# Optimization experiments

Measured on AMD Instinct MI355X. Metric: run time of the kernel, lower is better.

The kernel has to match this reference:

```python
import jax, jax.numpy as jnp
import numpy as np

B, C, H, W = 16, 512, 64, 64
R = 8
CP = C // R  # inner channel dim C' = 64


def setup_inputs() -> dict:
    key = jax.random.key(0)
    ks = jax.random.split(key, 10)
    s_in = 1.0 / np.sqrt(C)
    s_cp = 1.0 / np.sqrt(CP)
    return {
        "x": jax.random.normal(ks[0], (B, C, H, W), dtype=jnp.float32),
        "wq": jax.random.uniform(ks[1], (CP, C), jnp.float32, -s_in, s_in),
        "bq": jax.random.uniform(ks[2], (CP,), jnp.float32, -s_in, s_in),
        "wk": jax.random.uniform(ks[3], (CP, C), jnp.float32, -s_in, s_in),
        "bk": jax.random.uniform(ks[4], (CP,), jnp.float32, -s_in, s_in),
        "wv": jax.random.uniform(ks[5], (CP, C), jnp.float32, -s_in, s_in),
        "bv": jax.random.uniform(ks[6], (CP,), jnp.float32, -s_in, s_in),
        "wo": jax.random.uniform(ks[7], (C, CP), jnp.float32, -s_cp, s_cp),
        "bo": jax.random.uniform(ks[8], (C,), jnp.float32, -s_cp, s_cp),
        # torch init is gamma=0 (output==x, zero grads to convs); use small
        # nonzero value so the reference exercises the full graph.
        "gamma": jax.random.normal(ks[9], (1,), dtype=jnp.float32) * 0.1,
    }


def reference(x, wq, bq, wk, bk, wv, bv, wo, bo, gamma):
    b, c, h, w = x.shape
    n = h * w
    xf = x.reshape(b, c, n)  # flatten spatial -> (B, C, N)
    # 1x1 convs == channel matmuls
    q = jnp.einsum("oc,bcn->bon", wq, xf) + bq[:, None]  # (B, C', N)
    k = jnp.einsum("oc,bcn->bon", wk, xf) + bk[:, None]  # (B, C', N)
    v = jnp.einsum("oc,bcn->bon", wv, xf) + bv[:, None]  # (B, C', N)
    # energy = bmm(key (B,C',N), query^T (B,N,C')) -> (B, C', C')
    energy = jnp.einsum("bin,bjn->bij", k, q)
    attention = jax.nn.softmax(energy, axis=-1)  # (B, C', C')
    out = jnp.einsum("bij,bjn->bin", attention, v)  # (B, C', N)
    out = jnp.einsum("co,bon->bcn", wo, out) + bo[:, None]  # (B, C, N)
    out = out.reshape(b, c, h, w)
    return gamma * out + x
```

## Files before the change

kernel.cpp:

```cpp
#include <hip/hip_runtime.h>
#include <hip/hip_bf16.h>


#define NN 4096
#define CIN 512
#define CPD 64

typedef short s8v __attribute__((ext_vector_type(8)));
typedef float f4v __attribute__((ext_vector_type(4)));

__device__ __forceinline__ unsigned short f2bf(float f) {
    union { float f; unsigned int u; } c; c.f = f;
    unsigned int r = c.u + 0x7FFFu + ((c.u >> 16) & 1u);
    return (unsigned short)(r >> 16);
}

__global__ __launch_bounds__(512, 2) void k_qkv(
    const float* __restrict__ x,
    const float* __restrict__ wq, const float* __restrict__ bq,
    const float* __restrict__ wk, const float* __restrict__ bk,
    const float* __restrict__ wv, const float* __restrict__ bv,
    unsigned short* __restrict__ q, unsigned short* __restrict__ k,
    unsigned short* __restrict__ vt)
{
    const int nb = blockIdx.x, b = blockIdx.y;
    const int t = threadIdx.x;
    const int wv_ = t >> 6, L = t & 63, quad = L >> 4, l15 = L & 15;
    const int swz = (l15 & 7) * 8;

    __shared__ unsigned short wl[3][64 * 128];

    const float* wptr[3] = { wq, wk, wv };

    f4v acc[3][4][2];
    #pragma unroll
    for (int p = 0; p < 3; ++p)
        #pragma unroll
        for (int ot = 0; ot < 4; ++ot)
            #pragma unroll
            for (int nn = 0; nn < 2; ++nn) acc[p][ot][nn] = (f4v){0.f,0.f,0.f,0.f};

    const int n_col0 = nb * 256 + wv_ * 32 + l15;
    const size_t xbase = (size_t)b * CIN * NN;

    for (int cc = 0; cc < 4; ++cc) {
        __syncthreads();
        {
            const int o   = t & 63;
            const int c16 = (t >> 6) * 16;
            const int osw = (o & 7) * 8;
            #pragma unroll
            for (int p = 0; p < 3; ++p) {
                const float* wp = wptr[p] + (size_t)o * CIN + cc * 128 + c16;
                unsigned short tmp[16];
                #pragma unroll
                for (int f = 0; f < 4; ++f) {
                    float4 v = *(const float4*)(wp + f * 4);
                    tmp[f*4+0] = f2bf(v.x); tmp[f*4+1] = f2bf(v.y);
                    tmp[f*4+2] = f2bf(v.z); tmp[f*4+3] = f2bf(v.w);
                }
                #pragma unroll
                for (int u = 0; u < 2; ++u)
                    *(uint4*)&wl[p][o * 128 + ((c16 + u * 8) ^ osw)] =
                        *(const uint4*)&tmp[u * 8];
            }
        }
        __syncthreads();

        #pragma unroll
        for (int ksl = 0; ksl < 4; ++ksl) {
            const int c = cc * 128 + ksl * 32 + quad * 8;
            float bx0[8], bx1[8];
            #pragma unroll
            for (int j = 0; j < 8; ++j) {
                const float* xc = x + xbase + (size_t)(c + j) * NN + n_col0;
                bx0[j] = xc[0];
                bx1[j] = xc[16];
            }
            s8v bf0, bf1;
            #pragma unroll
            for (int j = 0; j < 8; ++j) {
                bf0[j] = (short)f2bf(bx0[j]);
                bf1[j] = (short)f2bf(bx1[j]);
            }
            const int cfrag = (ksl * 32 + quad * 8) ^ swz;
            #pragma unroll
            for (int p = 0; p < 3; ++p)
                #pragma unroll
                for (int ot = 0; ot < 4; ++ot) {
                    s8v af = *(const s8v*)&wl[p][(ot * 16 + l15) * 128 + cfrag];
                    acc[p][ot][0] = __builtin_amdgcn_mfma_f32_16x16x32_bf16(
                        af, bf0, acc[p][ot][0], 0, 0, 0);
                    acc[p][ot][1] = __builtin_amdgcn_mfma_f32_16x16x32_bf16(
                        af, bf1, acc[p][ot][1], 0, 0, 0);
                }
        }
    }

    const float* biasp[3] = { bq, bk, bv };
    #pragma unroll
    for (int p = 0; p < 2; ++p) {
        unsigned short* outp = ((p == 0) ? q : k) + (size_t)b * CPD * NN;
        #pragma unroll
        for (int ot = 0; ot < 4; ++ot) {
            float4 b4 = *(const float4*)(biasp[p] + ot * 16 + quad * 4);
            const float bsv[4] = { b4.x, b4.y, b4.z, b4.w };
            #pragma unroll
            for (int nn = 0; nn < 2; ++nn) {
                const int n = n_col0 + nn * 16;
                #pragma unroll
                for (int r = 0; r < 4; ++r) {
                    int o = ot * 16 + quad * 4 + r;
                    outp[(size_t)o * NN + n] = f2bf(acc[p][ot][nn][r] + bsv[r]);
                }
            }
        }
    }
    {
        unsigned short* vtb = vt + (size_t)b * NN * CPD;
        #pragma unroll
        for (int ot = 0; ot < 4; ++ot) {
            float4 b4 = *(const float4*)(bv + ot * 16 + quad * 4);
            const float bsv[4] = { b4.x, b4.y, b4.z, b4.w };
            #pragma unroll
            for (int nn = 0; nn < 2; ++nn) {
                const int n = n_col0 + nn * 16;
                unsigned short tmp[4];
                #pragma unroll
                for (int r = 0; r < 4; ++r) tmp[r] = f2bf(acc[2][ot][nn][r] + bsv[r]);
                *(uint2*)(vtb + (size_t)n * CPD + ot * 16 + quad * 4) = *(const uint2*)tmp;
            }
        }
    }
}

__global__ __launch_bounds__(256) void k_energy(
    const unsigned short* __restrict__ q, const unsigned short* __restrict__ k,
    float* __restrict__ epart)
{
    const int s = blockIdx.x;
    const int b = blockIdx.y;
    const int t = threadIdx.x;
    const int wv_ = t >> 6, L = t & 63, quad = L >> 4, l15 = L & 15;
    const unsigned short* kb = k + (size_t)b * CPD * NN;
    const unsigned short* qb = q + (size_t)b * CPD * NN;

    __shared__ float red[64 * 65];

    f4v acc[4][4];
    #pragma unroll
    for (int a = 0; a < 4; ++a)
        #pragma unroll
        for (int d = 0; d < 4; ++d) acc[a][d] = (f4v){0.f,0.f,0.f,0.f};

    const int nbase = s * 512 + wv_ * 128;
    #pragma unroll
    for (int ks = 0; ks < 4; ++ks) {
        const int n = nbase + ks * 32 + quad * 8;
        s8v af[4], bf_[4];
        #pragma unroll
        for (int it = 0; it < 4; ++it)
            af[it] = *(const s8v*)(kb + (size_t)(it * 16 + l15) * NN + n);
        #pragma unroll
        for (int jt = 0; jt < 4; ++jt)
            bf_[jt] = *(const s8v*)(qb + (size_t)(jt * 16 + l15) * NN + n);
        #pragma unroll
        for (int it = 0; it < 4; ++it)
            #pragma unroll
            for (int jt = 0; jt < 4; ++jt)
                acc[it][jt] = __builtin_amdgcn_mfma_f32_16x16x32_bf16(
                    af[it], bf_[jt], acc[it][jt], 0, 0, 0);
    }

    for (int idx = t; idx < 64 * 65; idx += 256) red[idx] = 0.f;
    __syncthreads();
    #pragma unroll
    for (int it = 0; it < 4; ++it)
        #pragma unroll
        for (int jt = 0; jt < 4; ++jt)
            #pragma unroll
            for (int r = 0; r < 4; ++r)
                atomicAdd(&red[(it * 16 + quad * 4 + r) * 65 + jt * 16 + l15],
                          acc[it][jt][r]);
    __syncthreads();
    float* ep = epart + ((size_t)b * 8 + s) * 4096;
    for (int idx = t; idx < 4096; idx += 256)
        ep[idx] = red[(idx >> 6) * 65 + (idx & 63)];
}

__global__ __launch_bounds__(64) void k_softmax(
    const float* __restrict__ epart, unsigned short* __restrict__ attn)
{
    const int i = blockIdx.x;
    const int b = blockIdx.y;
    const int j = threadIdx.x;
    float s = 0.f;
    #pragma unroll
    for (int sp = 0; sp < 8; ++sp)
        s += epart[((size_t)b * 8 + sp) * 4096 + i * 64 + j];
    float m = s;
    #pragma unroll
    for (int off = 32; off; off >>= 1) m = fmaxf(m, __shfl_xor(m, off));
    float e = __expf(s - m);
    float tot = e;
    #pragma unroll
    for (int off = 32; off; off >>= 1) tot += __shfl_xor(tot, off);
    attn[(size_t)b * 4096 + i * 64 + j] = f2bf(e / tot);
}

__global__ __launch_bounds__(256) void k_avout(
    const unsigned short* __restrict__ vt, const unsigned short* __restrict__ attn,
    const float* __restrict__ wo, const float* __restrict__ bo,
    const float* __restrict__ gamma, const float* __restrict__ x,
    float* __restrict__ out)
{
    const int nb = blockIdx.x, b = blockIdx.y;
    const int t = threadIdx.x;
    const int wv_ = t >> 6, L = t & 63, quad = L >> 4, l15 = L & 15;
    const int swz = (l15 & 7) * 8;

    __shared__ unsigned short wol[512 * 64];
    __shared__ unsigned short avl[128 * 64];

    {
        const int i16 = (t & 3) * 16;
        #pragma unroll
        for (int pass = 0; pass < 8; ++pass) {
            const int c = (t >> 2) + pass * 64;
            const int csw = (c & 7) * 8;
            const float* wp = wo + (size_t)c * CPD + i16;
            unsigned short tmp[16];
            #pragma unroll
            for (int f = 0; f < 4; ++f) {
                float4 v = *(const float4*)(wp + f * 4);
                tmp[f*4+0] = f2bf(v.x); tmp[f*4+1] = f2bf(v.y);
                tmp[f*4+2] = f2bf(v.z); tmp[f*4+3] = f2bf(v.w);
            }
            #pragma unroll
            for (int u = 0; u < 2; ++u)
                *(uint4*)&wol[c * 64 + ((i16 + u * 8) ^ csw)] = *(const uint4*)&tmp[u*8];
        }
    }

    {
        const unsigned short* ab  = attn + (size_t)b * 4096;
        const unsigned short* vtb = vt + (size_t)b * NN * CPD;
        const int n0 = nb * 128;
        f4v acc1[4][2];
        #pragma unroll
        for (int a = 0; a < 4; ++a)
            #pragma unroll
            for (int d = 0; d < 2; ++d) acc1[a][d] = (f4v){0.f,0.f,0.f,0.f};
        #pragma unroll
        for (int ks = 0; ks < 2; ++ks) {
            const int j = ks * 32 + quad * 8;
            s8v af[4], bf_[2];
            #pragma unroll
            for (int it = 0; it < 4; ++it)
                af[it] = *(const s8v*)(ab + (size_t)(it * 16 + l15) * 64 + j);
            #pragma unroll
            for (int nn = 0; nn < 2; ++nn)
                bf_[nn] = *(const s8v*)(vtb +
                    (size_t)(n0 + wv_ * 32 + nn * 16 + l15) * CPD + j);
            #pragma unroll
            for (int it = 0; it < 4; ++it)
                #pragma unroll
                for (int nn = 0; nn < 2; ++nn)
                    acc1[it][nn] = __builtin_amdgcn_mfma_f32_16x16x32_bf16(
                        af[it], bf_[nn], acc1[it][nn], 0, 0, 0);
        }
        #pragma unroll
        for (int it = 0; it < 4; ++it)
            #pragma unroll
            for (int nn = 0; nn < 2; ++nn) {
                const int nloc = wv_ * 32 + nn * 16 + l15;
                unsigned short tmp[4];
                #pragma unroll
                for (int r = 0; r < 4; ++r) tmp[r] = f2bf(acc1[it][nn][r]);
                *(uint2*)&avl[nloc * 64 + ((it * 16 + quad * 4) ^ swz)] =
                    *(const uint2*)tmp;
            }
    }
    __syncthreads();

    const float g = gamma[0];
    const int n0 = nb * 128;
    for (int cb = 0; cb < 8; ++cb) {
        f4v acc2[2][4];
        #pragma unroll
        for (int a = 0; a < 2; ++a)
            #pragma unroll
            for (int d = 0; d < 4; ++d) acc2[a][d] = (f4v){0.f,0.f,0.f,0.f};
        #pragma unroll
        for (int ks = 0; ks < 2; ++ks) {
            const int ic = (ks * 32 + quad * 8) ^ swz;
            s8v af2[2], bf2[4];
            #pragma unroll
            for (int nt = 0; nt < 2; ++nt)
                af2[nt] = *(const s8v*)&avl[(wv_ * 32 + nt * 16 + l15) * 64 + ic];
            #pragma unroll
            for (int ct = 0; ct < 4; ++ct)
                bf2[ct] = *(const s8v*)&wol[(cb * 64 + ct * 16 + l15) * 64 + ic];
            #pragma unroll
            for (int nt = 0; nt < 2; ++nt)
                #pragma unroll
                for (int ct = 0; ct < 4; ++ct)
                    acc2[nt][ct] = __builtin_amdgcn_mfma_f32_16x16x32_bf16(
                        af2[nt], bf2[ct], acc2[nt][ct], 0, 0, 0);
        }
        #pragma unroll
        for (int nt = 0; nt < 2; ++nt)
            #pragma unroll
            for (int ct = 0; ct < 4; ++ct) {
                const int c = cb * 64 + ct * 16 + l15;
                const float bs = bo[c];
                const int nbase = n0 + wv_ * 32 + nt * 16 + quad * 4;
                const size_t idx = ((size_t)b * CIN + c) * NN + nbase;
                float4 xr = *(const float4*)(x + idx);
                float4 r4;
                r4.x = g * (acc2[nt][ct][0] + bs) + xr.x;
                r4.y = g * (acc2[nt][ct][1] + bs) + xr.y;
                r4.z = g * (acc2[nt][ct][2] + bs) + xr.z;
                r4.w = g * (acc2[nt][ct][3] + bs) + xr.w;
                *(float4*)(out + idx) = r4;
            }
    }
}

extern "C" void kernel_launch(void* const* d_in, const int* in_sizes, int n_in,
                              void* d_out, int out_size, void* d_ws, size_t ws_size,
                              hipStream_t stream) {
    const float* x  = (const float*)d_in[0];
    const float* wq = (const float*)d_in[1];
    const float* bq = (const float*)d_in[2];
    const float* wk = (const float*)d_in[3];
    const float* bk = (const float*)d_in[4];
    const float* wv = (const float*)d_in[5];
    const float* bv = (const float*)d_in[6];
    const float* wo = (const float*)d_in[7];
    const float* bo = (const float*)d_in[8];
    const float* gm = (const float*)d_in[9];
    float* out = (float*)d_out;

    char* wsb = (char*)d_ws;
    unsigned short* q     = (unsigned short*)wsb;
    unsigned short* k     = (unsigned short*)(wsb + 8388608);
    unsigned short* vt    = (unsigned short*)(wsb + 16777216);
    float*          epart = (float*)(wsb + 25165824);
    unsigned short* attn  = (unsigned short*)(wsb + 27262976);

    k_qkv<<<dim3(16, 16), 512, 0, stream>>>(x, wq, bq, wk, bk, wv, bv, q, k, vt);
    k_energy<<<dim3(8, 16), 256, 0, stream>>>(q, k, epart);
    k_softmax<<<dim3(64, 16), 64, 0, stream>>>(epart, attn);
    k_avout<<<dim3(32, 16), 256, 0, stream>>>(vt, attn, wo, bo, gm, x, out);
}
```

Baseline: 341.0 us.

## Pre-convert weights to bf16 once and drop LDS staging in GEMM kernels

Adds a prep kernel that converts wq/wk/wv/wo to bf16 in workspace, so k_qkv and k_avout read bf16 weights straight from global/L2 and no longer convert and stage them in shared memory. k_qkv uses 256-thread blocks covering 128 columns with all 12 output tiles per wave, which doubles the grid and removes the block-level syncs. k_energy uses more, smaller blocks and writes per-wave partials with no LDS atomics, and softmax now sums 64 partials. The cost is an extra launch, more partial-sum traffic (a 16MB epart), and uncoalesced weight fragment loads from global memory.

```diff
diff --git a/kernel.cpp b/kernel.cpp
--- a/kernel.cpp
+++ b/kernel.cpp
@@ -1,5 +1,4 @@
 #include <hip/hip_runtime.h>
-#include <hip/hip_bf16.h>
 
 
 #define NN 4096
@@ -8,243 +7,203 @@
 
 typedef short s8v __attribute__((ext_vector_type(8)));
 typedef float f4v __attribute__((ext_vector_type(4)));
-
-__device__ __forceinline__ unsigned short f2bf(float f) {
+typedef unsigned short u16;
+
+__device__ __forceinline__ u16 f2bf(float f) {
     union { float f; unsigned int u; } c; c.f = f;
     unsigned int r = c.u + 0x7FFFu + ((c.u >> 16) & 1u);
-    return (unsigned short)(r >> 16);
-}
-
-__global__ __launch_bounds__(512, 2) void k_qkv(
+    return (u16)(r >> 16);
+}
+
+__global__ __launch_bounds__(256) void k_prep(
+    const float* __restrict__ wq, const float* __restrict__ wk,
+    const float* __restrict__ wv, const float* __restrict__ wo,
+    u16* __restrict__ wqkvb, u16* __restrict__ wob)
+{
+    const int t = blockIdx.x * 256 + threadIdx.x;
+    const int i4 = t * 4;
+    const float* src; u16* dst; int off;
+    if (i4 < 98304) {
+        const int r = i4 >> 15;
+        src = (r == 0) ? wq : (r == 1) ? wk : wv;
+        off = i4 & 32767;
+        dst = wqkvb + (r << 15);
+    } else {
+        src = wo; off = i4 - 98304; dst = wob;
+    }
+    float4 v = *(const float4*)(src + off);
+    u16 tmp[4] = { f2bf(v.x), f2bf(v.y), f2bf(v.z), f2bf(v.w) };
+    *(uint2*)(dst + off) = *(const uint2*)tmp;
+}
+
+__global__ __launch_bounds__(256, 2) void k_qkv(
     const float* __restrict__ x,
-    const float* __restrict__ wq, const float* __restrict__ bq,
-    const float* __restrict__ wk, const float* __restrict__ bk,
-    const float* __restrict__ wv, const float* __restrict__ bv,
-    unsigned short* __restrict__ q, unsigned short* __restrict__ k,
-    unsigned short* __restrict__ vt)
+    const u16* __restrict__ wqkvb,
+    const float* __restrict__ bq, const float* __restrict__ bk,
+    const float* __restrict__ bv,
+    u16* __restrict__ q, u16* __restrict__ k, u16* __restrict__ vt)
+{
+    const int nb = blockIdx.x, b = blockIdx.y;
+    const int t = threadIdx.x;
+    const int wv_ = t >> 6, L = t & 63, quad = L >> 4, l15 = L & 15;
+
+    const int n_col0 = nb * 128 + wv_ * 32 + l15;
+    const size_t xbase = (size_t)b * CIN * NN;
+
+    f4v acc[12][2];
+    #pragma unroll
+    for (int ot = 0; ot < 12; ++ot)
+        #pragma unroll
+        for (int nn = 0; nn < 2; ++nn) acc[ot][nn] = (f4v){0.f,0.f,0.f,0.f};
+
+    for (int ks = 0; ks < 16; ++ks) {
+        const int c = ks * 32 + quad * 8;
+        float bx0[8], bx1[8];
+        #pragma unroll
+        for (int j = 0; j < 8; ++j) {
+            const float* xc = x + xbase + (size_t)(c + j) * NN + n_col0;
+            bx0[j] = xc[0];
+            bx1[j] = xc[16];
+        }
+        s8v bf0, bf1;
+        #pragma unroll
+        for (int j = 0; j < 8; ++j) {
+            bf0[j] = (short)f2bf(bx0[j]);
+            bf1[j] = (short)f2bf(bx1[j]);
+        }
+        #pragma unroll
+        for (int ot = 0; ot < 12; ++ot) {
+            s8v af = *(const s8v*)(wqkvb + (ot * 16 + l15) * CIN + c);
+            acc[ot][0] = __builtin_amdgcn_mfma_f32_16x16x32_bf16(
+                af, bf0, acc[ot][0], 0, 0, 0);
+            acc[ot][1] = __builtin_amdgcn_mfma_f32_16x16x32_bf16(
+                af, bf1, acc[ot][1], 0, 0, 0);
+        }
+    }
+
+    #pragma unroll
+    for (int p = 0; p < 2; ++p) {
+        u16* outp = ((p == 0) ? q : k) + (size_t)b * CPD * NN;
+        const float* bp = (p == 0) ? bq : bk;
+        #pragma unroll
+        for (int ot4 = 0; ot4 < 4; ++ot4) {
+            float4 b4 = *(const float4*)(bp + ot4 * 16 + quad * 4);
+            const float bsv[4] = { b4.x, b4.y, b4.z, b4.w };
+            #pragma unroll
+            for (int nn = 0; nn < 2; ++nn) {
+                const int n = n_col0 + nn * 16;
+                #pragma unroll
+                for (int r = 0; r < 4; ++r) {
+                    int o = ot4 * 16 + quad * 4 + r;
+                    outp[(size_t)o * NN + n] =
+                        f2bf(acc[p * 4 + ot4][nn][r] + bsv[r]);
+                }
+            }
+        }
+    }
+    {
+        u16* vtb = vt + (size_t)b * NN * CPD;
+        #pragma unroll
+        for (int ot4 = 0; ot4 < 4; ++ot4) {
+            float4 b4 = *(const float4*)(bv + ot4 * 16 + quad * 4);
+            const float bsv[4] = { b4.x, b4.y, b4.z, b4.w };
+            #pragma unroll
+            for (int nn = 0; nn < 2; ++nn) {
+                const int n = n_col0 + nn * 16;
+                u16 tmp[4];
+                #pragma unroll
+                for (int r = 0; r < 4; ++r)
+                    tmp[r] = f2bf(acc[8 + ot4][nn][r] + bsv[r]);
+                *(uint2*)(vtb + (size_t)n * CPD + ot4 * 16 + quad * 4) =
+                    *(const uint2*)tmp;
+            }
+        }
+    }
+}
+
+__global__ __launch_bounds__(256, 4) void k_energy(
+    const u16* __restrict__ q, const u16* __restrict__ k,
+    float* __restrict__ epart)
+{
+    const int s = blockIdx.x;
+    const int b = blockIdx.y;
+    const int t = threadIdx.x;
+    const int wv_ = t >> 6, L = t & 63, quad = L >> 4, l15 = L & 15;
+    const u16* kb = k + (size_t)b * CPD * NN;
+    const u16* qb = q + (size_t)b * CPD * NN;
+
+    f4v acc[4][4];
+    #pragma unroll
+    for (int a = 0; a < 4; ++a)
+        #pragma unroll
+        for (int d = 0; d < 4; ++d) acc[a][d] = (f4v){0.f,0.f,0.f,0.f};
+
+    const int nbase = s * 256 + wv_ * 64;
+    #pragma unroll
+    for (int ksl = 0; ksl < 2; ++ksl) {
+        const int n = nbase + ksl * 32 + quad * 8;
+        s8v af[4], bf_[4];
+        #pragma unroll
+        for (int it = 0; it < 4; ++it)
+            af[it] = *(const s8v*)(kb + (size_t)(it * 16 + l15) * NN + n);
+        #pragma unroll
+        for (int jt = 0; jt < 4; ++jt)
+            bf_[jt] = *(const s8v*)(qb + (size_t)(jt * 16 + l15) * NN + n);
+        #pragma unroll
+        for (int it = 0; it < 4; ++it)
+            #pragma unroll
+            for (int jt = 0; jt < 4; ++jt)
+                acc[it][jt] = __builtin_amdgcn_mfma_f32_16x16x32_bf16(
+                    af[it], bf_[jt], acc[it][jt], 0, 0, 0);
+    }
+
+    float* ep = epart + ((size_t)b * 64 + s * 4 + wv_) * 4096;
+    #pragma unroll
+    for (int it = 0; it < 4; ++it)
+        #pragma unroll
+        for (int jt = 0; jt < 4; ++jt)
+            #pragma unroll
+            for (int r = 0; r < 4; ++r)
+                ep[(it * 16 + quad * 4 + r) * 64 + jt * 16 + l15] =
+                    acc[it][jt][r];
+}
+
+__global__ __launch_bounds__(64) void k_softmax(
+    const float* __restrict__ epart, u16* __restrict__ attn)
+{
+    const int i = blockIdx.x;
+    const int b = blockIdx.y;
+    const int j = threadIdx.x;
+    float s = 0.f;
+    #pragma unroll
+    for (int sp = 0; sp < 64; ++sp)
+        s += epart[((size_t)b * 64 + sp) * 4096 + i * 64 + j];
+    float m = s;
+    #pragma unroll
+    for (int off = 32; off; off >>= 1) m = fmaxf(m, __shfl_xor(m, off));
+    float e = __expf(s - m);
+    float tot = e;
+    #pragma unroll
+    for (int off = 32; off; off >>= 1) tot += __shfl_xor(tot, off);
+    attn[(size_t)b * 4096 + i * 64 + j] = f2bf(e / tot);
+}
+
+__global__ __launch_bounds__(256, 4) void k_avout(
+    const u16* __restrict__ vt, const u16* __restrict__ attn,
+    const u16* __restrict__ wob, const float* __restrict__ bo,
+    const float* __restrict__ gamma, const float* __restrict__ x,
+    float* __restrict__ out)
 {
     const int nb = blockIdx.x, b = blockIdx.y;
     const int t = threadIdx.x;
     const int wv_ = t >> 6, L = t & 63, quad = L >> 4, l15 = L & 15;
     const int swz = (l15 & 7) * 8;
 
-    __shared__ unsigned short wl[3][64 * 128];
-
-    const float* wptr[3] = { wq, wk, wv };
-
-    f4v acc[3][4][2];
-    #pragma unroll
-    for (int p = 0; p < 3; ++p)
-        #pragma unroll
-        for (int ot = 0; ot < 4; ++ot)
-            #pragma unroll
-            for (int nn = 0; nn < 2; ++nn) acc[p][ot][nn] = (f4v){0.f,0.f,0.f,0.f};
-
-    const int n_col0 = nb * 256 + wv_ * 32 + l15;
-    const size_t xbase = (size_t)b * CIN * NN;
-
-    for (int cc = 0; cc < 4; ++cc) {
-        __syncthreads();
-        {
-            const int o   = t & 63;
-            const int c16 = (t >> 6) * 16;
-            const int osw = (o & 7) * 8;
-            #pragma unroll
-            for (int p = 0; p < 3; ++p) {
-                const float* wp = wptr[p] + (size_t)o * CIN + cc * 128 + c16;
-                unsigned short tmp[16];
-                #pragma unroll
-                for (int f = 0; f < 4; ++f) {
-                    float4 v = *(const float4*)(wp + f * 4);
-                    tmp[f*4+0] = f2bf(v.x); tmp[f*4+1] = f2bf(v.y);
-                    tmp[f*4+2] = f2bf(v.z); tmp[f*4+3] = f2bf(v.w);
-                }
-                #pragma unroll
-                for (int u = 0; u < 2; ++u)
-                    *(uint4*)&wl[p][o * 128 + ((c16 + u * 8) ^ osw)] =
-                        *(const uint4*)&tmp[u * 8];
-            }
-        }
-        __syncthreads();
-
-        #pragma unroll
-        for (int ksl = 0; ksl < 4; ++ksl) {
-            const int c = cc * 128 + ksl * 32 + quad * 8;
-            float bx0[8], bx1[8];
-            #pragma unroll
-            for (int j = 0; j < 8; ++j) {
-                const float* xc = x + xbase + (size_t)(c + j) * NN + n_col0;
-                bx0[j] = xc[0];
-                bx1[j] = xc[16];
-            }
-            s8v bf0, bf1;
-            #pragma unroll
-            for (int j = 0; j < 8; ++j) {
-                bf0[j] = (short)f2bf(bx0[j]);
-                bf1[j] = (short)f2bf(bx1[j]);
-            }
-            const int cfrag = (ksl * 32 + quad * 8) ^ swz;
-            #pragma unroll
-            for (int p = 0; p < 3; ++p)
-                #pragma unroll
-                for (int ot = 0; ot < 4; ++ot) {
-                    s8v af = *(const s8v*)&wl[p][(ot * 16 + l15) * 128 + cfrag];
-                    acc[p][ot][0] = __builtin_amdgcn_mfma_f32_16x16x32_bf16(
-                        af, bf0, acc[p][ot][0], 0, 0, 0);
-                    acc[p][ot][1] = __builtin_amdgcn_mfma_f32_16x16x32_bf16(
-                        af, bf1, acc[p][ot][1], 0, 0, 0);
-                }
-        }
-    }
-
-    const float* biasp[3] = { bq, bk, bv };
-    #pragma unroll
-    for (int p = 0; p < 2; ++p) {
-        unsigned short* outp = ((p == 0) ? q : k) + (size_t)b * CPD * NN;
-        #pragma unroll
-        for (int ot = 0; ot < 4; ++ot) {
-            float4 b4 = *(const float4*)(biasp[p] + ot * 16 + quad * 4);
-            const float bsv[4] = { b4.x, b4.y, b4.z, b4.w };
-            #pragma unroll
-            for (int nn = 0; nn < 2; ++nn) {
-                const int n = n_col0 + nn * 16;
-                #pragma unroll
-                for (int r = 0; r < 4; ++r) {
-                    int o = ot * 16 + quad * 4 + r;
-                    outp[(size_t)o * NN + n] = f2bf(acc[p][ot][nn][r] + bsv[r]);
-                }
-            }
-        }
-    }
+    __shared__ u16 avl[128 * 64];
+
     {
-        unsigned short* vtb = vt + (size_t)b * NN * CPD;
-        #pragma unroll
-        for (int ot = 0; ot < 4; ++ot) {
-            float4 b4 = *(const float4*)(bv + ot * 16 + quad * 4);
-            const float bsv[4] = { b4.x, b4.y, b4.z, b4.w };
-            #pragma unroll
-            for (int nn = 0; nn < 2; ++nn) {
-                const int n = n_col0 + nn * 16;
-                unsigned short tmp[4];
-                #pragma unroll
-                for (int r = 0; r < 4; ++r) tmp[r] = f2bf(acc[2][ot][nn][r] + bsv[r]);
-                *(uint2*)(vtb + (size_t)n * CPD + ot * 16 + quad * 4) = *(const uint2*)tmp;
-            }
-        }
-    }
-}
-
-__global__ __launch_bounds__(256) void k_energy(
-    const unsigned short* __restrict__ q, const unsigned short* __restrict__ k,
-    float* __restrict__ epart)
-{
-    const int s = blockIdx.x;
-    const int b = blockIdx.y;
-    const int t = threadIdx.x;
-    const int wv_ = t >> 6, L = t & 63, quad = L >> 4, l15 = L & 15;
-    const unsigned short* kb = k + (size_t)b * CPD * NN;
-    const unsigned short* qb = q + (size_t)b * CPD * NN;
-
-    __shared__ float red[64 * 65];
-
-    f4v acc[4][4];
-    #pragma unroll
-    for (int a = 0; a < 4; ++a)
-        #pragma unroll
-        for (int d = 0; d < 4; ++d) acc[a][d] = (f4v){0.f,0.f,0.f,0.f};
-
-    const int nbase = s * 512 + wv_ * 128;
-    #pragma unroll
-    for (int ks = 0; ks < 4; ++ks) {
-        const int n = nbase + ks * 32 + quad * 8;
-        s8v af[4], bf_[4];
-        #pragma unroll
-        for (int it = 0; it < 4; ++it)
-            af[it] = *(const s8v*)(kb + (size_t)(it * 16 + l15) * NN + n);
-        #pragma unroll
-        for (int jt = 0; jt < 4; ++jt)
-            bf_[jt] = *(const s8v*)(qb + (size_t)(jt * 16 + l15) * NN + n);
-        #pragma unroll
-        for (int it = 0; it < 4; ++it)
-            #pragma unroll
-            for (int jt = 0; jt < 4; ++jt)
-                acc[it][jt] = __builtin_amdgcn_mfma_f32_16x16x32_bf16(
-                    af[it], bf_[jt], acc[it][jt], 0, 0, 0);
-    }
-
-    for (int idx = t; idx < 64 * 65; idx += 256) red[idx] = 0.f;
-    __syncthreads();
-    #pragma unroll
-    for (int it = 0; it < 4; ++it)
-        #pragma unroll
-        for (int jt = 0; jt < 4; ++jt)
-            #pragma unroll
-            for (int r = 0; r < 4; ++r)
-                atomicAdd(&red[(it * 16 + quad * 4 + r) * 65 + jt * 16 + l15],
-                          acc[it][jt][r]);
-    __syncthreads();
-    float* ep = epart + ((size_t)b * 8 + s) * 4096;
-    for (int idx = t; idx < 4096; idx += 256)
-        ep[idx] = red[(idx >> 6) * 65 + (idx & 63)];
-}
-
-__global__ __launch_bounds__(64) void k_softmax(
-    const float* __restrict__ epart, unsigned short* __restrict__ attn)
-{
-    const int i = blockIdx.x;
-    const int b = blockIdx.y;
-    const int j = threadIdx.x;
-    float s = 0.f;
-    #pragma unroll
-    for (int sp = 0; sp < 8; ++sp)
-        s += epart[((size_t)b * 8 + sp) * 4096 + i * 64 + j];
-    float m = s;
-    #pragma unroll
-    for (int off = 32; off; off >>= 1) m = fmaxf(m, __shfl_xor(m, off));
-    float e = __expf(s - m);
-    float tot = e;
-    #pragma unroll
-    for (int off = 32; off; off >>= 1) tot += __shfl_xor(tot, off);
-    attn[(size_t)b * 4096 + i * 64 + j] = f2bf(e / tot);
-}
-
-__global__ __launch_bounds__(256) void k_avout(
-    const unsigned short* __restrict__ vt, const unsigned short* __restrict__ attn,
-    const float* __restrict__ wo, const float* __restrict__ bo,
-    const float* __restrict__ gamma, const float* __restrict__ x,
-    float* __restrict__ out)
-{
-    const int nb = blockIdx.x, b = blockIdx.y;
-    const int t = threadIdx.x;
-    const int wv_ = t >> 6, L = t & 63, quad = L >> 4, l15 = L & 15;
-    const int swz = (l15 & 7) * 8;
-
-    __shared__ unsigned short wol[512 * 64];
-    __shared__ unsigned short avl[128 * 64];
-
-    {
-        const int i16 = (t & 3) * 16;
-        #pragma unroll
-        for (int pass = 0; pass < 8; ++pass) {
-            const int c = (t >> 2) + pass * 64;
-            const int csw = (c & 7) * 8;
-            const float* wp = wo + (size_t)c * CPD + i16;
-            unsigned short tmp[16];
-            #pragma unroll
-            for (int f = 0; f < 4; ++f) {
-                float4 v = *(const float4*)(wp + f * 4);
-                tmp[f*4+0] = f2bf(v.x); tmp[f*4+1] = f2bf(v.y);
-                tmp[f*4+2] = f2bf(v.z); tmp[f*4+3] = f2bf(v.w);
-            }
-            #pragma unroll
-            for (int u = 0; u < 2; ++u)
-                *(uint4*)&wol[c * 64 + ((i16 + u * 8) ^ csw)] = *(const uint4*)&tmp[u*8];
-        }
-    }
-
-    {
-        const unsigned short* ab  = attn + (size_t)b * 4096;
-        const unsigned short* vtb = vt + (size_t)b * NN * CPD;
+        const u16* ab  = attn + (size_t)b * 4096;
+        const u16* vtb = vt + (size_t)b * NN * CPD;
         const int n0 = nb * 128;
         f4v acc1[4][2];
         #pragma unroll
@@ -274,7 +233,7 @@
             #pragma unroll
             for (int nn = 0; nn < 2; ++nn) {
                 const int nloc = wv_ * 32 + nn * 16 + l15;
-                unsigned short tmp[4];
+                u16 tmp[4];
                 #pragma unroll
                 for (int r = 0; r < 4; ++r) tmp[r] = f2bf(acc1[it][nn][r]);
                 *(uint2*)&avl[nloc * 64 + ((it * 16 + quad * 4) ^ swz)] =
@@ -293,14 +252,16 @@
             for (int d = 0; d < 4; ++d) acc2[a][d] = (f4v){0.f,0.f,0.f,0.f};
         #pragma unroll
         for (int ks = 0; ks < 2; ++ks) {
-            const int ic = (ks * 32 + quad * 8) ^ swz;
+            const int i0 = ks * 32 + quad * 8;
+            const int ic = i0 ^ swz;
             s8v af2[2], bf2[4];
             #pragma unroll
             for (int nt = 0; nt < 2; ++nt)
                 af2[nt] = *(const s8v*)&avl[(wv_ * 32 + nt * 16 + l15) * 64 + ic];
             #pragma unroll
             for (int ct = 0; ct < 4; ++ct)
-                bf2[ct] = *(const s8v*)&wol[(cb * 64 + ct * 16 + l15) * 64 + ic];
+                bf2[ct] = *(const s8v*)(wob +
+                    (size_t)(cb * 64 + ct * 16 + l15) * CPD + i0);
             #pragma unroll
             for (int nt = 0; nt < 2; ++nt)
                 #pragma unroll
@@ -343,14 +304,17 @@
     float* out = (float*)d_out;
 
     char* wsb = (char*)d_ws;
-    unsigned short* q     = (unsigned short*)wsb;
-    unsigned short* k     = (unsigned short*)(wsb + 8388608);
-    unsigned short* vt    = (unsigned short*)(wsb + 16777216);
-    float*          epart = (float*)(wsb + 25165824);
-    unsigned short* attn  = (unsigned short*)(wsb + 27262976);
-
-    k_qkv<<<dim3(16, 16), 512, 0, stream>>>(x, wq, bq, wk, bk, wv, bv, q, k, vt);
-    k_energy<<<dim3(8, 16), 256, 0, stream>>>(q, k, epart);
+    u16*   q     = (u16*)wsb;
+    u16*   k     = (u16*)(wsb + 8388608);
+    u16*   vt    = (u16*)(wsb + 16777216);
+    float* epart = (float*)(wsb + 25165824);
+    u16*   attn  = (u16*)(wsb + 41943040);
+    u16*   wqkvb = (u16*)(wsb + 42074112);
+    u16*   wob   = (u16*)(wsb + 42270720);
+
+    k_prep<<<128, 256, 0, stream>>>(wq, wk, wv, wo, wqkvb, wob);
+    k_qkv<<<dim3(32, 16), 256, 0, stream>>>(x, wqkvb, bq, bk, bv, q, k, vt);
+    k_energy<<<dim3(16, 16), 256, 0, stream>>>(q, k, epart);
     k_softmax<<<dim3(64, 16), 64, 0, stream>>>(epart, attn);
-    k_avout<<<dim3(32, 16), 256, 0, stream>>>(vt, attn, wo, bo, gm, x, out);
-}
+    k_avout<<<dim3(32, 16), 256, 0, stream>>>(vt, attn, wob, bo, gm, x, out);
+}
```

Measured after the change: 355.4 us. 4.2% more time.
